# Kernel tuning notes

Hardware: AMD Instinct MI355X
Metric: run time of the kernel (lower is better)

Reference implementation:

```python
import jax, jax.numpy as jnp
import numpy as np

TEMPERATURE = 0.07
BASE_TEMPERATURE = 0.07
L_MAX = 16  # max number of session labels per dialogue
NEG_INF = -1e30


def setup_inputs() -> dict:
    key = jax.random.key(0)
    k1, k2, k3 = jax.random.split(key, 3)
    B, T, H = 128, 1024, 256
    features = jax.random.normal(k1, (B, T, H), dtype=jnp.float32)
    dialogue_lengths = jax.random.randint(k2, (B,), 1, T + 1)
    labels = jax.random.randint(k3, (B, T), 0, L_MAX)
    return {"features": features, "dialogue_lengths": dialogue_lengths, "labels": labels}


def reference(features, dialogue_lengths, labels):
    B, T, H = features.shape
    valid = jnp.arange(T)[None, :] < dialogue_lengths[:, None]            # [B,T]
    # one-hot label assignment, zeroed at padded positions
    oh = (labels[..., None] == jnp.arange(L_MAX)[None, None, :]) & valid[..., None]
    ohf = oh.astype(features.dtype)                                       # [B,T,L]
    counts = ohf.sum(axis=1)                                              # [B,L]
    # per-dialogue, per-label prototype = mean of member features
    proto_sum = jnp.einsum('btl,bth->blh', ohf, features)                 # [B,L,H]
    prototypes = proto_sum / jnp.maximum(counts, 1.0)[..., None]          # [B,L,H]
    # anchor-vs-prototype logits
    logits = jnp.einsum('bth,blh->btl', features, prototypes) / TEMPERATURE
    present = counts > 0                                                  # [B,L]
    logits = jnp.where(present[:, None, :], logits, NEG_INF)
    log_prob = jax.nn.log_softmax(logits, axis=-1)                        # [B,T,L]
    # mask is one-hot on each token's own label -> mean_log_prob_pos is log_prob at own label
    pos = jnp.take_along_axis(log_prob, labels[..., None], axis=-1)[..., 0]  # [B,T]
    tok_loss = -(TEMPERATURE / BASE_TEMPERATURE) * pos
    per_dialogue = jnp.sum(jnp.where(valid, tok_loss, 0.0), axis=1) / dialogue_lengths.astype(features.dtype)
    return per_dialogue.mean()
```

## Files before the change

kernel.cpp:

```cpp
#include <hip/hip_runtime.h>
#include <math.h>

#define B 128
#define T 1024
#define H 256
#define L 16
#define INV_TEMP (1.0f/0.07f)
#define NEG_INF -1e30f


__global__ __launch_bounds__(256) void proto_kernel(
    const float* __restrict__ feat, const int* __restrict__ dlen,
    const int* __restrict__ labels, float* __restrict__ ws_pp,
    int* __restrict__ ws_cntp, float* __restrict__ out) {
  __shared__ float acc[4][L * 128];
  __shared__ int labs[256];
  __shared__ int cnt[L];

  const int bx = blockIdx.x;
  if (bx == 0 && threadIdx.x == 0) out[0] = 0.f;

  const int b = bx >> 3;
  const int chunk = (bx >> 2) & 1;
  const int seg = bx & 3;
  const int tid = threadIdx.x;
  const int w = tid >> 6;
  const int lane = tid & 63;

  const int len = dlen[b];
  if (seg * 256 >= len) return;

  for (int i = tid; i < 4 * L * 128; i += 256) ((float*)acc)[i] = 0.f;
  labs[tid] = labels[(size_t)b * T + seg * 256 + tid];
  if (tid < L) cnt[tid] = 0;
  __syncthreads();

  if (chunk == 0 && (seg * 256 + tid) < len) atomicAdd(&cnt[labs[tid]], 1);

  int nt = len - seg * 256 - w * 64;
  if (nt > 64) nt = 64;
  const float2* fbase = (const float2*)(feat +
      ((size_t)b * T + seg * 256 + w * 64) * H + chunk * 128);
  float* a = acc[w];

  int j = 0;
  for (; j + 4 <= nt; j += 4) {
    float2 f0 = fbase[(size_t)(j + 0) * (H / 2) + lane];
    float2 f1 = fbase[(size_t)(j + 1) * (H / 2) + lane];
    float2 f2 = fbase[(size_t)(j + 2) * (H / 2) + lane];
    float2 f3 = fbase[(size_t)(j + 3) * (H / 2) + lane];
    const int l0 = labs[w * 64 + j + 0];
    const int l1 = labs[w * 64 + j + 1];
    const int l2 = labs[w * 64 + j + 2];
    const int l3 = labs[w * 64 + j + 3];
    float2* p0 = (float2*)&a[l0 * 128 + lane * 2];
    { float2 v = *p0; v.x += f0.x; v.y += f0.y; *p0 = v; }
    float2* p1 = (float2*)&a[l1 * 128 + lane * 2];
    { float2 v = *p1; v.x += f1.x; v.y += f1.y; *p1 = v; }
    float2* p2 = (float2*)&a[l2 * 128 + lane * 2];
    { float2 v = *p2; v.x += f2.x; v.y += f2.y; *p2 = v; }
    float2* p3 = (float2*)&a[l3 * 128 + lane * 2];
    { float2 v = *p3; v.x += f3.x; v.y += f3.y; *p3 = v; }
  }
  for (; j < nt; ++j) {
    float2 f = fbase[(size_t)j * (H / 2) + lane];
    const int lab = labs[w * 64 + j];
    float2* p = (float2*)&a[lab * 128 + lane * 2];
    float2 v = *p; v.x += f.x; v.y += f.y; *p = v;
  }
  __syncthreads();

  float* op = ws_pp + (((size_t)b * 4 + seg) * L) * H + chunk * 128;
  for (int e = tid; e < L * 128; e += 256) {
    const float s = acc[0][e] + acc[1][e] + acc[2][e] + acc[3][e];
    op[(e >> 7) * H + (e & 127)] = s;
  }
  if (chunk == 0 && tid < L) ws_cntp[(b * 4 + seg) * L + tid] = cnt[tid];
}

__global__ __launch_bounds__(256) void dotsloss_kernel(
    const float* __restrict__ feat, const int* __restrict__ dlen,
    const int* __restrict__ labels, const float* __restrict__ ws_pp,
    const int* __restrict__ ws_cntp, float* __restrict__ out) {
  __shared__ float pr[L * H];
  __shared__ int cnts[L];
  __shared__ float red[256];

  const int b = blockIdx.x >> 2;
  const int seg = blockIdx.x & 3;
  const int tid = threadIdx.x;

  const int len = dlen[b];
  if (seg * 256 >= len) return;
  const int nseg = (len + 255) >> 8;

  if (tid < L) {
    const int* cp = ws_cntp + b * 4 * L + tid;
    int c = 0;
    for (int s = 0; s < nseg; ++s) c += cp[s * L];
    cnts[tid] = c;
  }
  __syncthreads();

  const float* gp = ws_pp + (size_t)b * 4 * L * H;
  for (int i = tid; i < L * H; i += 256) {
    const int l = i >> 8;
    float s = 0.f;
    for (int sg = 0; sg < nseg; ++sg) s += gp[(sg * L + l) * H + (i & (H - 1))];
    const int cn = cnts[l];
    pr[i] = s * (cn > 0 ? 1.f / (float)cn : 0.f);
  }
  __syncthreads();

  const int t = seg * 256 + tid;
  float tok = 0.f;

  if (t < len) {
    const float4* f4 = (const float4*)(feat + ((size_t)b * T + t) * H);
    float dot[L];
#pragma unroll
    for (int l = 0; l < L; ++l) dot[l] = 0.f;

#pragma unroll 4
    for (int cb = 0; cb < 16; ++cb) {
      float4 f[4];
#pragma unroll
      for (int q = 0; q < 4; ++q) f[q] = f4[cb * 4 + q];
#pragma unroll
      for (int q = 0; q < 4; ++q) {
#pragma unroll
        for (int l = 0; l < L; ++l) {
          const float4 p = *(const float4*)&pr[l * H + cb * 16 + q * 4];
          dot[l] += f[q].x * p.x + f[q].y * p.y +
                    f[q].z * p.z + f[q].w * p.w;
        }
      }
    }

    float lg[L];
#pragma unroll
    for (int l = 0; l < L; ++l)
      lg[l] = (cnts[l] > 0) ? dot[l] * INV_TEMP : NEG_INF;
    float m = lg[0];
#pragma unroll
    for (int l = 1; l < L; ++l) m = fmaxf(m, lg[l]);
    float se = 0.f;
#pragma unroll
    for (int l = 0; l < L; ++l) se += expf(lg[l] - m);
    const float lsp = m + logf(se);

    const int lab = labels[(size_t)b * T + t];
    float pos = 0.f;
#pragma unroll
    for (int l = 0; l < L; ++l) pos += (l == lab) ? lg[l] : 0.f;

    tok = lsp - pos;
  }

  red[tid] = tok;
  __syncthreads();
#pragma unroll
  for (int s = 128; s > 0; s >>= 1) {
    if (tid < s) red[tid] += red[tid + s];
    __syncthreads();
  }
  if (tid == 0) atomicAdd(out, red[0] / ((float)len * (float)B));
}

extern "C" void kernel_launch(void* const* d_in, const int* in_sizes, int n_in,
                              void* d_out, int out_size, void* d_ws, size_t ws_size,
                              hipStream_t stream) {
  const float* feat = (const float*)d_in[0];
  const int* dlen = (const int*)d_in[1];
  const int* labels = (const int*)d_in[2];
  float* out = (float*)d_out;

  float* ws_pp = (float*)d_ws;
  int* ws_cntp = (int*)(ws_pp + (size_t)B * 4 * L * H);

  proto_kernel<<<B * 8, 256, 0, stream>>>(feat, dlen, labels, ws_pp, ws_cntp, out);
  dotsloss_kernel<<<B * 4, 256, 0, stream>>>(feat, dlen, labels, ws_pp, ws_cntp, out);
}
```

Before: 238.0 us.

## Fuse prototype and loss kernels into one cooperative kernel with grid sync

Merges the two kernels into a single persistent cooperative kernel of 512 blocks. Each block loops over the work units of both phases, and a grid-wide sync separates them. This removes a kernel launch and the gap between launches, and may keep features warm in cache. In exchange it adds the cost of the grid barrier and reduces parallelism per phase, with a fallback to the two-kernel path if the cooperative launch fails.

```diff
diff --git a/kernel.cpp b/kernel.cpp
--- a/kernel.cpp
+++ b/kernel.cpp
@@ -1,4 +1,5 @@
 #include <hip/hip_runtime.h>
+#include <hip/hip_cooperative_groups.h>
 #include <math.h>
 
 #define B 128
@@ -7,7 +8,167 @@
 #define L 16
 #define INV_TEMP (1.0f/0.07f)
 #define NEG_INF -1e30f
-
+#define GRID_FUSED 512
+
+namespace cg = cooperative_groups;
+
+
+__global__ __launch_bounds__(256, 2) void fused_kernel(
+    const float* __restrict__ feat, const int* __restrict__ dlen,
+    const int* __restrict__ labels, float* __restrict__ ws_pp,
+    int* __restrict__ ws_cntp, float* __restrict__ out) {
+  __shared__ float acc[4][L * 128];
+  __shared__ int labs[256];
+  __shared__ int cnts[L];
+  __shared__ float red[256];
+
+  const int tid = threadIdx.x;
+  if (blockIdx.x == 0 && tid == 0) out[0] = 0.f;
+
+  for (int u = blockIdx.x; u < B * 8; u += GRID_FUSED) {
+    const int b = u >> 3;
+    const int chunk = (u >> 2) & 1;
+    const int seg = u & 3;
+    const int len = dlen[b];
+    if (seg * 256 >= len) continue;
+
+    const int w = tid >> 6;
+    const int lane = tid & 63;
+
+    for (int i = tid; i < 4 * L * 128; i += 256) ((float*)acc)[i] = 0.f;
+    labs[tid] = labels[(size_t)b * T + seg * 256 + tid];
+    if (tid < L) cnts[tid] = 0;
+    __syncthreads();
+
+    if (chunk == 0 && (seg * 256 + tid) < len) atomicAdd(&cnts[labs[tid]], 1);
+
+    int nt = len - seg * 256 - w * 64;
+    if (nt > 64) nt = 64;
+    const float2* fbase = (const float2*)(feat +
+        ((size_t)b * T + seg * 256 + w * 64) * H + chunk * 128);
+    float* a = acc[w];
+
+    int j = 0;
+    for (; j + 4 <= nt; j += 4) {
+      float2 f0 = fbase[(size_t)(j + 0) * (H / 2) + lane];
+      float2 f1 = fbase[(size_t)(j + 1) * (H / 2) + lane];
+      float2 f2 = fbase[(size_t)(j + 2) * (H / 2) + lane];
+      float2 f3 = fbase[(size_t)(j + 3) * (H / 2) + lane];
+      const int l0 = labs[w * 64 + j + 0];
+      const int l1 = labs[w * 64 + j + 1];
+      const int l2 = labs[w * 64 + j + 2];
+      const int l3 = labs[w * 64 + j + 3];
+      float2* p0 = (float2*)&a[l0 * 128 + lane * 2];
+      { float2 v = *p0; v.x += f0.x; v.y += f0.y; *p0 = v; }
+      float2* p1 = (float2*)&a[l1 * 128 + lane * 2];
+      { float2 v = *p1; v.x += f1.x; v.y += f1.y; *p1 = v; }
+      float2* p2 = (float2*)&a[l2 * 128 + lane * 2];
+      { float2 v = *p2; v.x += f2.x; v.y += f2.y; *p2 = v; }
+      float2* p3 = (float2*)&a[l3 * 128 + lane * 2];
+      { float2 v = *p3; v.x += f3.x; v.y += f3.y; *p3 = v; }
+    }
+    for (; j < nt; ++j) {
+      float2 f = fbase[(size_t)j * (H / 2) + lane];
+      const int lab = labs[w * 64 + j];
+      float2* p = (float2*)&a[lab * 128 + lane * 2];
+      float2 v = *p; v.x += f.x; v.y += f.y; *p = v;
+    }
+    __syncthreads();
+
+    float* op = ws_pp + (((size_t)b * 4 + seg) * L) * H + chunk * 128;
+    for (int e = tid; e < L * 128; e += 256) {
+      const float s = acc[0][e] + acc[1][e] + acc[2][e] + acc[3][e];
+      op[(e >> 7) * H + (e & 127)] = s;
+    }
+    if (chunk == 0 && tid < L) ws_cntp[(b * 4 + seg) * L + tid] = cnts[tid];
+    __syncthreads();
+  }
+
+  cg::this_grid().sync();
+
+  float* pr = &acc[0][0];
+  for (int u = blockIdx.x; u < B * 4; u += GRID_FUSED) {
+    const int b = u >> 2;
+    const int seg = u & 3;
+    const int len = dlen[b];
+    if (seg * 256 >= len) continue;
+    const int nseg = (len + 255) >> 8;
+
+    if (tid < L) {
+      const int* cp = ws_cntp + b * 4 * L + tid;
+      int c = 0;
+      for (int s = 0; s < nseg; ++s) c += cp[s * L];
+      cnts[tid] = c;
+    }
+    __syncthreads();
+
+    const float* gp = ws_pp + (size_t)b * 4 * L * H;
+    for (int i = tid; i < L * H; i += 256) {
+      const int l = i >> 8;
+      float s = 0.f;
+      for (int sg = 0; sg < nseg; ++sg)
+        s += gp[(sg * L + l) * H + (i & (H - 1))];
+      const int cn = cnts[l];
+      pr[i] = s * (cn > 0 ? 1.f / (float)cn : 0.f);
+    }
+    __syncthreads();
+
+    const int t = seg * 256 + tid;
+    float tok = 0.f;
+
+    if (t < len) {
+      const float4* f4 = (const float4*)(feat + ((size_t)b * T + t) * H);
+      float dot[L];
+#pragma unroll
+      for (int l = 0; l < L; ++l) dot[l] = 0.f;
+
+#pragma unroll 4
+      for (int cb = 0; cb < 16; ++cb) {
+        float4 f[4];
+#pragma unroll
+        for (int q = 0; q < 4; ++q) f[q] = f4[cb * 4 + q];
+#pragma unroll
+        for (int q = 0; q < 4; ++q) {
+#pragma unroll
+          for (int l = 0; l < L; ++l) {
+            const float4 p = *(const float4*)&pr[l * H + cb * 16 + q * 4];
+            dot[l] += f[q].x * p.x + f[q].y * p.y +
+                      f[q].z * p.z + f[q].w * p.w;
+          }
+        }
+      }
+
+      float lg[L];
+#pragma unroll
+      for (int l = 0; l < L; ++l)
+        lg[l] = (cnts[l] > 0) ? dot[l] * INV_TEMP : NEG_INF;
+      float m = lg[0];
+#pragma unroll
+      for (int l = 1; l < L; ++l) m = fmaxf(m, lg[l]);
+      float se = 0.f;
+#pragma unroll
+      for (int l = 0; l < L; ++l) se += expf(lg[l] - m);
+      const float lsp = m + logf(se);
+
+      const int lab = labels[(size_t)b * T + t];
+      float pos = 0.f;
+#pragma unroll
+      for (int l = 0; l < L; ++l) pos += (l == lab) ? lg[l] : 0.f;
+
+      tok = lsp - pos;
+    }
+
+    red[tid] = tok;
+    __syncthreads();
+#pragma unroll
+    for (int s = 128; s > 0; s >>= 1) {
+      if (tid < s) red[tid] += red[tid + s];
+      __syncthreads();
+    }
+    if (tid == 0) atomicAdd(out, red[0] / ((float)len * (float)B));
+    __syncthreads();
+  }
+}
 
 __global__ __launch_bounds__(256) void proto_kernel(
     const float* __restrict__ feat, const int* __restrict__ dlen,
@@ -178,6 +339,14 @@
   float* ws_pp = (float*)d_ws;
   int* ws_cntp = (int*)(ws_pp + (size_t)B * 4 * L * H);
 
-  proto_kernel<<<B * 8, 256, 0, stream>>>(feat, dlen, labels, ws_pp, ws_cntp, out);
-  dotsloss_kernel<<<B * 4, 256, 0, stream>>>(feat, dlen, labels, ws_pp, ws_cntp, out);
+  void* args[] = {(void*)&feat, (void*)&dlen, (void*)&labels,
+                  (void*)&ws_pp, (void*)&ws_cntp, (void*)&out};
+  hipError_t err = hipLaunchCooperativeKernel(
+      fused_kernel, dim3(GRID_FUSED), dim3(256), args, 0, stream);
+  if (err != hipSuccess) {
+    proto_kernel<<<B * 8, 256, 0, stream>>>(feat, dlen, labels, ws_pp,
+                                            ws_cntp, out);
+    dotsloss_kernel<<<B * 4, 256, 0, stream>>>(feat, dlen, labels, ws_pp,
+                                               ws_cntp, out);
+  }
 }
```

Measured after the change: 317.0 us. 33.2% more time.

## Bucket tokens by label for register-accumulated prototypes; split H across threads in dots

Applied to the files above, without the earlier changes.

The prototype kernel now builds per-label token index lists in shared memory. Each thread (one label, one float4 column slice) then gathers member rows and accumulates them in registers, replacing the shared-memory read-modify-write scatter. It launches 16 blocks per dialogue instead of 8. The loss kernel has each thread compute partial dots for two tokens over half of H and combine them through shared memory, which lowers register and LDS pressure per token and vectorises the prototype reduction. A risk is that padded tokens past len now have their features read and dot products computed, so some wasted bandwidth remains.

```diff
diff --git a/kernel.cpp b/kernel.cpp
--- a/kernel.cpp
+++ b/kernel.cpp
@@ -13,69 +13,58 @@
     const float* __restrict__ feat, const int* __restrict__ dlen,
     const int* __restrict__ labels, float* __restrict__ ws_pp,
     int* __restrict__ ws_cntp, float* __restrict__ out) {
-  __shared__ float acc[4][L * 128];
-  __shared__ int labs[256];
+  __shared__ int idx[L][256];
   __shared__ int cnt[L];
 
   const int bx = blockIdx.x;
   if (bx == 0 && threadIdx.x == 0) out[0] = 0.f;
 
-  const int b = bx >> 3;
-  const int chunk = (bx >> 2) & 1;
-  const int seg = bx & 3;
+  const int b = bx >> 4;
+  const int seg = (bx >> 2) & 3;
+  const int ch = bx & 3;
   const int tid = threadIdx.x;
-  const int w = tid >> 6;
-  const int lane = tid & 63;
 
   const int len = dlen[b];
   if (seg * 256 >= len) return;
-
-  for (int i = tid; i < 4 * L * 128; i += 256) ((float*)acc)[i] = 0.f;
-  labs[tid] = labels[(size_t)b * T + seg * 256 + tid];
+  int segLen = len - seg * 256;
+  if (segLen > 256) segLen = 256;
+
   if (tid < L) cnt[tid] = 0;
   __syncthreads();
-
-  if (chunk == 0 && (seg * 256 + tid) < len) atomicAdd(&cnt[labs[tid]], 1);
-
-  int nt = len - seg * 256 - w * 64;
-  if (nt > 64) nt = 64;
-  const float2* fbase = (const float2*)(feat +
-      ((size_t)b * T + seg * 256 + w * 64) * H + chunk * 128);
-  float* a = acc[w];
-
-  int j = 0;
-  for (; j + 4 <= nt; j += 4) {
-    float2 f0 = fbase[(size_t)(j + 0) * (H / 2) + lane];
-    float2 f1 = fbase[(size_t)(j + 1) * (H / 2) + lane];
-    float2 f2 = fbase[(size_t)(j + 2) * (H / 2) + lane];
-    float2 f3 = fbase[(size_t)(j + 3) * (H / 2) + lane];
-    const int l0 = labs[w * 64 + j + 0];
-    const int l1 = labs[w * 64 + j + 1];
-    const int l2 = labs[w * 64 + j + 2];
-    const int l3 = labs[w * 64 + j + 3];
-    float2* p0 = (float2*)&a[l0 * 128 + lane * 2];
-    { float2 v = *p0; v.x += f0.x; v.y += f0.y; *p0 = v; }
-    float2* p1 = (float2*)&a[l1 * 128 + lane * 2];
-    { float2 v = *p1; v.x += f1.x; v.y += f1.y; *p1 = v; }
-    float2* p2 = (float2*)&a[l2 * 128 + lane * 2];
-    { float2 v = *p2; v.x += f2.x; v.y += f2.y; *p2 = v; }
-    float2* p3 = (float2*)&a[l3 * 128 + lane * 2];
-    { float2 v = *p3; v.x += f3.x; v.y += f3.y; *p3 = v; }
-  }
-  for (; j < nt; ++j) {
-    float2 f = fbase[(size_t)j * (H / 2) + lane];
-    const int lab = labs[w * 64 + j];
-    float2* p = (float2*)&a[lab * 128 + lane * 2];
-    float2 v = *p; v.x += f.x; v.y += f.y; *p = v;
-  }
-  __syncthreads();
-
-  float* op = ws_pp + (((size_t)b * 4 + seg) * L) * H + chunk * 128;
-  for (int e = tid; e < L * 128; e += 256) {
-    const float s = acc[0][e] + acc[1][e] + acc[2][e] + acc[3][e];
-    op[(e >> 7) * H + (e & 127)] = s;
-  }
-  if (chunk == 0 && tid < L) ws_cntp[(b * 4 + seg) * L + tid] = cnt[tid];
+  if (tid < segLen) {
+    const int l = labels[(size_t)b * T + seg * 256 + tid];
+    const int p = atomicAdd(&cnt[l], 1);
+    idx[l][p] = tid;
+  }
+  __syncthreads();
+
+  const int l = tid >> 4;
+  const int cs = tid & 15;
+  const float4* fb4 = (const float4*)feat +
+      ((size_t)b * T + seg * 256) * (H / 4) + ch * 16 + cs;
+
+  const int c = cnt[l];
+  float4 a = make_float4(0.f, 0.f, 0.f, 0.f);
+  int i = 0;
+  for (; i + 8 <= c; i += 8) {
+    int t8[8];
+#pragma unroll
+    for (int u = 0; u < 8; ++u) t8[u] = idx[l][i + u];
+    float4 f8[8];
+#pragma unroll
+    for (int u = 0; u < 8; ++u) f8[u] = fb4[(size_t)t8[u] * (H / 4)];
+#pragma unroll
+    for (int u = 0; u < 8; ++u) {
+      a.x += f8[u].x; a.y += f8[u].y; a.z += f8[u].z; a.w += f8[u].w;
+    }
+  }
+  for (; i < c; ++i) {
+    const float4 f = fb4[(size_t)idx[l][i] * (H / 4)];
+    a.x += f.x; a.y += f.y; a.z += f.z; a.w += f.w;
+  }
+
+  *(float4*)(ws_pp + (((size_t)b * 4 + seg) * L + l) * H + ch * 64 + cs * 4) = a;
+  if (ch == 0 && tid < L) ws_cntp[(b * 4 + seg) * L + tid] = cnt[tid];
 }
 
 __global__ __launch_bounds__(256) void dotsloss_kernel(
@@ -83,15 +72,16 @@
     const int* __restrict__ labels, const float* __restrict__ ws_pp,
     const int* __restrict__ ws_cntp, float* __restrict__ out) {
   __shared__ float pr[L * H];
+  __shared__ float part[256][L];
   __shared__ int cnts[L];
   __shared__ float red[256];
 
   const int b = blockIdx.x >> 2;
-  const int seg = blockIdx.x & 3;
+  const int q = blockIdx.x & 3;
   const int tid = threadIdx.x;
 
   const int len = dlen[b];
-  if (seg * 256 >= len) return;
+  if (q * 256 >= len) return;
   const int nseg = (len + 255) >> 8;
 
   if (tid < L) {
@@ -102,59 +92,90 @@
   }
   __syncthreads();
 
-  const float* gp = ws_pp + (size_t)b * 4 * L * H;
-  for (int i = tid; i < L * H; i += 256) {
-    const int l = i >> 8;
-    float s = 0.f;
-    for (int sg = 0; sg < nseg; ++sg) s += gp[(sg * L + l) * H + (i & (H - 1))];
+  const float4* gp4 = (const float4*)(ws_pp + (size_t)b * 4 * L * H);
+  for (int i = tid; i < L * H / 4; i += 256) {
+    const int l = i >> 6;
+    float4 s = gp4[i];
+    for (int sg = 1; sg < nseg; ++sg) {
+      const float4 t2 = gp4[sg * (L * 64) + i];
+      s.x += t2.x; s.y += t2.y; s.z += t2.z; s.w += t2.w;
+    }
     const int cn = cnts[l];
-    pr[i] = s * (cn > 0 ? 1.f / (float)cn : 0.f);
-  }
-  __syncthreads();
-
-  const int t = seg * 256 + tid;
+    const float inv = (cn > 0) ? 1.f / (float)cn : 0.f;
+    ((float4*)pr)[i] = make_float4(s.x * inv, s.y * inv, s.z * inv, s.w * inv);
+  }
+  __syncthreads();
+
+  const int ts = tid & 127;
+  const int hh = tid >> 7;
+  const int t0 = q * 256 + ts;
+  const int t1 = t0 + 128;
+
+  const float4* fA = (const float4*)feat + ((size_t)b * T + t0) * (H / 4) + hh * 32;
+  const float4* fB = (const float4*)feat + ((size_t)b * T + t1) * (H / 4) + hh * 32;
+
+  float dot0[L], dot1[L];
+#pragma unroll
+  for (int l = 0; l < L; ++l) { dot0[l] = 0.f; dot1[l] = 0.f; }
+
+#pragma unroll 2
+  for (int cb = 0; cb < 8; ++cb) {
+    float4 fa[4], fb_[4];
+#pragma unroll
+    for (int q4 = 0; q4 < 4; ++q4) {
+      fa[q4] = fA[cb * 4 + q4];
+      fb_[q4] = fB[cb * 4 + q4];
+    }
+#pragma unroll
+    for (int q4 = 0; q4 < 4; ++q4) {
+#pragma unroll
+      for (int l = 0; l < L; ++l) {
+        const float4 p = *(const float4*)&pr[l * H + hh * 128 + cb * 16 + q4 * 4];
+        dot0[l] += fa[q4].x * p.x + fa[q4].y * p.y +
+                   fa[q4].z * p.z + fa[q4].w * p.w;
+        dot1[l] += fb_[q4].x * p.x + fb_[q4].y * p.y +
+                   fb_[q4].z * p.z + fb_[q4].w * p.w;
+      }
+    }
+  }
+
+  if (hh == 1) {
+#pragma unroll
+    for (int l = 0; l < L; ++l) {
+      part[ts][l] = dot0[l];
+      part[ts + 128][l] = dot1[l];
+    }
+  }
+  __syncthreads();
+
   float tok = 0.f;
-
-  if (t < len) {
-    const float4* f4 = (const float4*)(feat + ((size_t)b * T + t) * H);
-    float dot[L];
-#pragma unroll
-    for (int l = 0; l < L; ++l) dot[l] = 0.f;
-
-#pragma unroll 4
-    for (int cb = 0; cb < 16; ++cb) {
-      float4 f[4];
-#pragma unroll
-      for (int q = 0; q < 4; ++q) f[q] = f4[cb * 4 + q];
-#pragma unroll
-      for (int q = 0; q < 4; ++q) {
+  if (hh == 0) {
+#pragma unroll
+    for (int k = 0; k < 2; ++k) {
+      const int t = t0 + k * 128;
+      if (t < len) {
+        float lg[L];
 #pragma unroll
         for (int l = 0; l < L; ++l) {
-          const float4 p = *(const float4*)&pr[l * H + cb * 16 + q * 4];
-          dot[l] += f[q].x * p.x + f[q].y * p.y +
-                    f[q].z * p.z + f[q].w * p.w;
+          const float d = (k == 0 ? dot0[l] : dot1[l]) + part[ts + k * 128][l];
+          lg[l] = (cnts[l] > 0) ? d * INV_TEMP : NEG_INF;
         }
+        float m = lg[0];
+#pragma unroll
+        for (int l = 1; l < L; ++l) m = fmaxf(m, lg[l]);
+        float se = 0.f;
+#pragma unroll
+        for (int l = 0; l < L; ++l) se += expf(lg[l] - m);
+        const float lsp = m + logf(se);
+
+        const int lab = labels[(size_t)b * T + t];
+        float pos = 0.f;
+#pragma unroll
+        for (int l = 0; l < L; ++l) pos += (l == lab) ? lg[l] : 0.f;
+
+        tok += lsp - pos;
       }
     }
-
-    float lg[L];
-#pragma unroll
-    for (int l = 0; l < L; ++l)
-      lg[l] = (cnts[l] > 0) ? dot[l] * INV_TEMP : NEG_INF;
-    float m = lg[0];
-#pragma unroll
-    for (int l = 1; l < L; ++l) m = fmaxf(m, lg[l]);
-    float se = 0.f;
-#pragma unroll
-    for (int l = 0; l < L; ++l) se += expf(lg[l] - m);
-    const float lsp = m + logf(se);
-
-    const int lab = labels[(size_t)b * T + t];
-    float pos = 0.f;
-#pragma unroll
-    for (int l = 0; l < L; ++l) pos += (l == lab) ? lg[l] : 0.f;
-
-    tok = lsp - pos;
   }
 
   red[tid] = tok;
@@ -178,6 +199,8 @@
   float* ws_pp = (float*)d_ws;
   int* ws_cntp = (int*)(ws_pp + (size_t)B * 4 * L * H);
 
-  proto_kernel<<<B * 8, 256, 0, stream>>>(feat, dlen, labels, ws_pp, ws_cntp, out);
-  dotsloss_kernel<<<B * 4, 256, 0, stream>>>(feat, dlen, labels, ws_pp, ws_cntp, out);
+  proto_kernel<<<B * 16, 256, 0, stream>>>(feat, dlen, labels, ws_pp,
+                                           ws_cntp, out);
+  dotsloss_kernel<<<B * 4, 256, 0, stream>>>(feat, dlen, labels, ws_pp,
+                                             ws_cntp, out);
 }
```

New measurement: 215.9 us. 9.3% less time.
